# Kernel tuning notes

Measured on AMD Instinct MI355X. Metric: run time of the kernel, lower is better.

The kernel has to match this reference:

```python
import jax, jax.numpy as jnp
import numpy as np

NUM_GRAPHS = 512

def gcn_conv(x, W, b, src, dst, num_nodes):
    # PyG GCNConv: h = x @ W; add self-loops; symmetric norm D^-1/2 A D^-1/2; + bias
    h = x @ W  # [N, F]
    ones = jnp.ones(src.shape[0], dtype=x.dtype)
    deg = jax.ops.segment_sum(ones, dst, num_segments=num_nodes) + 1.0  # +1 for self-loop
    dinv = jax.lax.rsqrt(deg)  # deg >= 1 always
    coef = dinv[src] * dinv[dst]  # [E]
    msg = h[src] * coef[:, None]  # [E, F]  (dominant memory traffic)
    agg = jax.ops.segment_sum(msg, dst, num_segments=num_nodes)
    agg = agg + h * (dinv * dinv)[:, None]  # self-loop term, norm = dinv_i^2
    return agg + b

def global_mean_pool(x, batch, num_graphs):
    s = jax.ops.segment_sum(x, batch, num_segments=num_graphs)
    cnt = jax.ops.segment_sum(jnp.ones(x.shape[0], dtype=x.dtype), batch, num_segments=num_graphs)
    return s / jnp.maximum(cnt, 1.0)[:, None]

def setup_inputs() -> dict:
    key = jax.random.key(0)
    ks = jax.random.split(key, 8)
    N, E, D, H, C = 100000, 3200000, 128, 64, 2
    x = jax.random.normal(ks[0], (N, D), dtype=jnp.float32)
    edge_index = jax.random.randint(ks[1], (2, E), 0, N, dtype=jnp.int32)
    batch = jnp.sort(jax.random.randint(ks[2], (N,), 0, NUM_GRAPHS, dtype=jnp.int32))
    W1 = jax.random.normal(ks[3], (D, H), dtype=jnp.float32) / np.sqrt(D)
    b1 = jnp.zeros((H,), dtype=jnp.float32)
    W2 = jax.random.normal(ks[4], (H, H), dtype=jnp.float32) / np.sqrt(H)
    b2 = jnp.zeros((H,), dtype=jnp.float32)
    Wlin = jax.random.normal(ks[5], (H, C), dtype=jnp.float32) / np.sqrt(H)
    blin = jnp.zeros((C,), dtype=jnp.float32)
    return {"x": x, "edge_index": edge_index, "batch": batch,
            "W1": W1, "b1": b1, "W2": W2, "b2": b2, "Wlin": Wlin, "blin": blin}

def reference(x, edge_index, batch, W1, b1, W2, b2, Wlin, blin):
    # Dropout is identity at inference; omitted for a deterministic reference.
    num_nodes = x.shape[0]
    src, dst = edge_index[0], edge_index[1]
    h = jax.nn.relu(gcn_conv(x, W1, b1, src, dst, num_nodes))
    h = jax.nn.relu(gcn_conv(h, W2, b2, src, dst, num_nodes))
    g = global_mean_pool(h, batch, NUM_GRAPHS)  # [G, H]
    return g @ Wlin + blin  # [G, 2]
```

## Files before the change

kernel.cpp:

```cpp
#include <hip/hip_runtime.h>

#define HF 64
typedef unsigned short bfraw;

__device__ __forceinline__ float bf2f(bfraw u) {
    return __uint_as_float((unsigned)u << 16);
}
__device__ __forceinline__ bfraw f2bf(float f) {
    unsigned u = __float_as_uint(f);
    unsigned r = (u + 0x7FFFu + ((u >> 16) & 1u)) >> 16;
    return (bfraw)r;
}

__global__ void hist_kernel(const int* __restrict__ dst, int* __restrict__ deg, int E) {
    int e = blockIdx.x * blockDim.x + threadIdx.x;
    if (e < E) atomicAdd(&deg[dst[e]], 1);
}

__global__ __launch_bounds__(256) void scan_partial(const int* __restrict__ deg,
                                                    int* __restrict__ blocksum, int N) {
    __shared__ int red[256];
    int base = blockIdx.x * 1024 + threadIdx.x * 4;
    int s = 0;
#pragma unroll
    for (int j = 0; j < 4; ++j) {
        int i = base + j;
        if (i < N) s += deg[i];
    }
    red[threadIdx.x] = s;
    __syncthreads();
    for (int o = 128; o > 0; o >>= 1) {
        if (threadIdx.x < o) red[threadIdx.x] += red[threadIdx.x + o];
        __syncthreads();
    }
    if (threadIdx.x == 0) blocksum[blockIdx.x] = red[0];
}

__global__ __launch_bounds__(256) void scan_blocksums(int* __restrict__ blocksum, int nb) {
    __shared__ int lds[256];
    int t = threadIdx.x;
    int v = (t < nb) ? blocksum[t] : 0;
    lds[t] = v;
    __syncthreads();
    for (int o = 1; o < 256; o <<= 1) {
        int add = (t >= o) ? lds[t - o] : 0;
        __syncthreads();
        lds[t] += add;
        __syncthreads();
    }
    if (t < nb) blocksum[t] = lds[t] - v;
}

__global__ __launch_bounds__(256) void scan_apply(const int* __restrict__ deg,
                                                  const int* __restrict__ blocksum,
                                                  int* __restrict__ cursor,
                                                  float* __restrict__ dinv, int N) {
    __shared__ int lds[256];
    int base = blockIdx.x * 1024 + threadIdx.x * 4;
    int v[4];
    int s = 0;
#pragma unroll
    for (int j = 0; j < 4; ++j) {
        int i = base + j;
        v[j] = (i < N) ? deg[i] : 0;
        s += v[j];
    }
    lds[threadIdx.x] = s;
    __syncthreads();
    for (int o = 1; o < 256; o <<= 1) {
        int add = (threadIdx.x >= o) ? lds[threadIdx.x - o] : 0;
        __syncthreads();
        lds[threadIdx.x] += add;
        __syncthreads();
    }
    int run = blocksum[blockIdx.x] + lds[threadIdx.x] - s;
#pragma unroll
    for (int j = 0; j < 4; ++j) {
        int i = base + j;
        if (i < N) {
            cursor[i] = run;
            dinv[i] = rsqrtf((float)v[j] + 1.0f);
            run += v[j];
        }
    }
}

__global__ void fill_kernel(const int* __restrict__ src, const int* __restrict__ dst,
                            int* __restrict__ cursor, int* __restrict__ csr_src, int E) {
    int e = blockIdx.x * blockDim.x + threadIdx.x;
    if (e < E) {
        int d = dst[e];
        int pos = atomicAdd(&cursor[d], 1);
        csr_src[pos] = src[e];
    }
}

template <int K>
__global__ __launch_bounds__(256) void gemm_scale_f32_kernel(const float* __restrict__ X,
                                                             const float* __restrict__ W,
                                                             const float* __restrict__ scale,
                                                             bfraw* __restrict__ Y, int N) {
    __shared__ float Wl[K * HF];
    __shared__ float xs[32 * K];
    for (int i = threadIdx.x; i < K * HF; i += 256) Wl[i] = W[i];

    int node0 = blockIdx.x * 32;
    const float4* X4 = (const float4*)(X + (size_t)node0 * K);
    float4* xs4 = (float4*)xs;
    int totalf4 = 32 * K / 4;
    for (int i = threadIdx.x; i < totalf4; i += 256) {
        int n = i / (K / 4);
        if (node0 + n < N) xs4[i] = X4[i];
    }
    __syncthreads();

    int wave = threadIdx.x >> 6, f = threadIdx.x & 63;
    for (int n = wave; n < 32; n += 4) {
        int node = node0 + n;
        if (node >= N) break;
        const float4* xr = (const float4*)&xs[n * K];
        float acc = 0.0f;
#pragma unroll
        for (int k4 = 0; k4 < K / 4; ++k4) {
            float4 xv = xr[k4];
            acc += xv.x * Wl[(k4 * 4 + 0) * HF + f];
            acc += xv.y * Wl[(k4 * 4 + 1) * HF + f];
            acc += xv.z * Wl[(k4 * 4 + 2) * HF + f];
            acc += xv.w * Wl[(k4 * 4 + 3) * HF + f];
        }
        Y[(size_t)node * HF + f] = f2bf(acc * scale[node]);
    }
}

__global__ __launch_bounds__(256) void gemm_scale_bf16_kernel(const bfraw* __restrict__ X,
                                                              const float* __restrict__ W,
                                                              const float* __restrict__ scale,
                                                              bfraw* __restrict__ Y, int N) {
    __shared__ float Wl[HF * HF];
    __shared__ float xs[32 * HF];
    for (int i = threadIdx.x; i < HF * HF; i += 256) Wl[i] = W[i];

    int node0 = blockIdx.x * 32;
    const ushort4* X4 = (const ushort4*)(X + (size_t)node0 * HF);
    for (int i = threadIdx.x; i < 32 * HF / 4; i += 256) {
        int n = i >> 4;
        if (node0 + n < N) {
            ushort4 u = X4[i];
            float4 fv = make_float4(bf2f(u.x), bf2f(u.y), bf2f(u.z), bf2f(u.w));
            ((float4*)xs)[i] = fv;
        }
    }
    __syncthreads();

    int wave = threadIdx.x >> 6, f = threadIdx.x & 63;
    for (int n = wave; n < 32; n += 4) {
        int node = node0 + n;
        if (node >= N) break;
        const float4* xr = (const float4*)&xs[n * HF];
        float acc = 0.0f;
#pragma unroll
        for (int k4 = 0; k4 < HF / 4; ++k4) {
            float4 xv = xr[k4];
            acc += xv.x * Wl[(k4 * 4 + 0) * HF + f];
            acc += xv.y * Wl[(k4 * 4 + 1) * HF + f];
            acc += xv.z * Wl[(k4 * 4 + 2) * HF + f];
            acc += xv.w * Wl[(k4 * 4 + 3) * HF + f];
        }
        Y[(size_t)node * HF + f] = f2bf(acc * scale[node]);
    }
}

__device__ __forceinline__ float edge_gather_sum(const bfraw* __restrict__ hs,
                                                 const int* __restrict__ csr_src,
                                                 int beg, int end, int f) {
    float acc = 0.0f;
    for (int base = beg; base < end; base += 32) {
        int li = base + (f & 31);
        int myidx = csr_src[li < end ? li : beg];
        int rem = end - base;
#pragma unroll
        for (int j = 0; j < 32; ++j) {
            int s = __builtin_amdgcn_readlane(myidx, j);
            float v = bf2f(hs[(size_t)s * HF + f]);
            acc += (j < rem) ? v : 0.0f;
        }
    }
    return acc;
}

__global__ __launch_bounds__(256) void agg_relu_kernel(const bfraw* __restrict__ hs,
                                                       const int* __restrict__ cursor,
                                                       const int* __restrict__ deg,
                                                       const int* __restrict__ csr_src,
                                                       const float* __restrict__ dinv,
                                                       const float* __restrict__ b,
                                                       bfraw* __restrict__ out, int N) {
    int d = blockIdx.x * 4 + (threadIdx.x >> 6);
    if (d >= N) return;
    int f = threadIdx.x & 63;
    int end = cursor[d];
    int beg = end - deg[d];
    float acc = edge_gather_sum(hs, csr_src, beg, end, f);
    float self = bf2f(hs[(size_t)d * HF + f]);
    float v = dinv[d] * (acc + self) + b[f];
    out[(size_t)d * HF + f] = f2bf(fmaxf(v, 0.0f));
}

__global__ __launch_bounds__(256) void agg_pool_kernel(const bfraw* __restrict__ hs,
                                                       const int* __restrict__ cursor,
                                                       const int* __restrict__ deg,
                                                       const int* __restrict__ csr_src,
                                                       const float* __restrict__ dinv,
                                                       const float* __restrict__ b,
                                                       const int* __restrict__ batch,
                                                       float* __restrict__ pool,
                                                       float* __restrict__ cnt, int N) {
    int d = blockIdx.x * 4 + (threadIdx.x >> 6);
    if (d >= N) return;
    int f = threadIdx.x & 63;
    int end = cursor[d];
    int beg = end - deg[d];
    float acc = edge_gather_sum(hs, csr_src, beg, end, f);
    float self = bf2f(hs[(size_t)d * HF + f]);
    float v = fmaxf(dinv[d] * (acc + self) + b[f], 0.0f);
    int g = batch[d];
    atomicAdd(&pool[g * HF + f], v);
    if (f == 0) atomicAdd(&cnt[g], 1.0f);
}

__global__ void final_kernel(const float* __restrict__ pool, const float* __restrict__ cnt,
                             const float* __restrict__ Wlin, const float* __restrict__ blin,
                             float* __restrict__ out) {
    int g = blockIdx.x;
    int f = threadIdx.x;
    float v = pool[g * HF + f] / fmaxf(cnt[g], 1.0f);
    float s0 = v * Wlin[f * 2 + 0];
    float s1 = v * Wlin[f * 2 + 1];
#pragma unroll
    for (int off = 32; off > 0; off >>= 1) {
        s0 += __shfl_down(s0, off);
        s1 += __shfl_down(s1, off);
    }
    if (f == 0) {
        out[g * 2 + 0] = s0 + blin[0];
        out[g * 2 + 1] = s1 + blin[1];
    }
}

extern "C" void kernel_launch(void* const* d_in, const int* in_sizes, int n_in,
                              void* d_out, int out_size, void* d_ws, size_t ws_size,
                              hipStream_t stream) {
    const float* x    = (const float*)d_in[0];
    const int*   ei   = (const int*)d_in[1];
    const int*   bat  = (const int*)d_in[2];
    const float* W1   = (const float*)d_in[3];
    const float* b1   = (const float*)d_in[4];
    const float* W2   = (const float*)d_in[5];
    const float* b2   = (const float*)d_in[6];
    const float* Wlin = (const float*)d_in[7];
    const float* blin = (const float*)d_in[8];

    const int N = in_sizes[2];
    const int E = in_sizes[1] / 2;
    const int G = out_size / 2;
    const int* src  = ei;
    const int* dstv = ei + E;

    int*   deg      = (int*)d_ws;
    int*   cursor   = deg + N;
    int*   blocksum = cursor + N;
    int*   csr_src  = blocksum + 256;
    float* dinv     = (float*)(csr_src + E);
    float* pool     = dinv + N;
    float* cnt      = pool + (size_t)G * HF;
    uintptr_t p = (uintptr_t)(cnt + G);
    p = (p + 15) & ~(uintptr_t)15;
    bfraw* bufT = (bfraw*)p;
    bfraw* bufH = bufT + (size_t)N * HF;

    int nb = (N + 1023) / 1024;

    hipMemsetAsync(deg, 0, (size_t)N * sizeof(int), stream);
    hist_kernel<<<(E + 255) / 256, 256, 0, stream>>>(dstv, deg, E);
    scan_partial<<<nb, 256, 0, stream>>>(deg, blocksum, N);
    scan_blocksums<<<1, 256, 0, stream>>>(blocksum, nb);
    scan_apply<<<nb, 256, 0, stream>>>(deg, blocksum, cursor, dinv, N);
    fill_kernel<<<(E + 255) / 256, 256, 0, stream>>>(src, dstv, cursor, csr_src, E);

    gemm_scale_f32_kernel<128><<<(N + 31) / 32, 256, 0, stream>>>(x, W1, dinv, bufT, N);
    agg_relu_kernel<<<(N + 3) / 4, 256, 0, stream>>>(bufT, cursor, deg, csr_src, dinv, b1,
                                                     bufH, N);

    gemm_scale_bf16_kernel<<<(N + 31) / 32, 256, 0, stream>>>(bufH, W2, dinv, bufT, N);
    hipMemsetAsync(pool, 0, ((size_t)G * HF + G) * sizeof(float), stream);
    agg_pool_kernel<<<(N + 3) / 4, 256, 0, stream>>>(bufT, cursor, deg, csr_src, dinv, b2,
                                                     bat, pool, cnt, N);

    final_kernel<<<G, HF, 0, stream>>>(pool, cnt, Wlin, blin, (float*)d_out);
}
```

Before: 976.5 us.

## Partition CSR fill by destination range and batch gather loads before summing

The CSR fill kernel now launches 8 groups of blocks. Each group reads every edge but only handles edges whose destination falls in its eighth of the node range. This keeps the atomics and scattered writes confined to a smaller address window, which should improve locality, probably in the XCD-local caches. In the aggregation gather, full 32-edge chunks now issue all 32 loads into a register array before accumulating, and the masked tail is split into its own path so more loads can be in flight. The cost is that dst is read 8 times in the fill, plus extra register pressure in the gather.

```diff
diff --git a/kernel.cpp b/kernel.cpp
--- a/kernel.cpp
+++ b/kernel.cpp
@@ -85,13 +85,21 @@
     }
 }
 
-__global__ void fill_kernel(const int* __restrict__ src, const int* __restrict__ dst,
-                            int* __restrict__ cursor, int* __restrict__ csr_src, int E) {
-    int e = blockIdx.x * blockDim.x + threadIdx.x;
-    if (e < E) {
+__global__ __launch_bounds__(256) void fill_kernel(const int* __restrict__ src,
+                                                   const int* __restrict__ dst,
+                                                   int* __restrict__ cursor,
+                                                   int* __restrict__ csr_src,
+                                                   int E, int part, int nblk) {
+    int p = blockIdx.x & 7;
+    int blk = blockIdx.x >> 3;
+    int plo = p * part;
+    int phi = plo + part;
+    for (int e = blk * 256 + threadIdx.x; e < E; e += nblk * 256) {
         int d = dst[e];
-        int pos = atomicAdd(&cursor[d], 1);
-        csr_src[pos] = src[e];
+        if (d >= plo && d < phi) {
+            int pos = atomicAdd(&cursor[d], 1);
+            csr_src[pos] = src[e];
+        }
     }
 }
 
@@ -174,16 +182,30 @@
                                                  const int* __restrict__ csr_src,
                                                  int beg, int end, int f) {
     float acc = 0.0f;
-    for (int base = beg; base < end; base += 32) {
-        int li = base + (f & 31);
-        int myidx = csr_src[li < end ? li : beg];
-        int rem = end - base;
+    int base = beg;
+    for (; base + 32 <= end; base += 32) {
+        int myidx = csr_src[base + (f & 31)];
+        float v[32];
 #pragma unroll
         for (int j = 0; j < 32; ++j) {
             int s = __builtin_amdgcn_readlane(myidx, j);
-            float v = bf2f(hs[(size_t)s * HF + f]);
-            acc += (j < rem) ? v : 0.0f;
-        }
+            v[j] = bf2f(hs[(size_t)s * HF + f]);
+        }
+#pragma unroll
+        for (int j = 0; j < 32; ++j) acc += v[j];
+    }
+    if (base < end) {
+        int li = base + (f & 31);
+        int myidx = csr_src[li < end ? li : base];
+        int rem = end - base;
+        float v[32];
+#pragma unroll
+        for (int j = 0; j < 32; ++j) {
+            int s = __builtin_amdgcn_readlane(myidx, j);
+            v[j] = bf2f(hs[(size_t)s * HF + f]);
+        }
+#pragma unroll
+        for (int j = 0; j < 32; ++j) acc += (j < rem) ? v[j] : 0.0f;
     }
     return acc;
 }
@@ -285,7 +307,9 @@
     scan_partial<<<nb, 256, 0, stream>>>(deg, blocksum, N);
     scan_blocksums<<<1, 256, 0, stream>>>(blocksum, nb);
     scan_apply<<<nb, 256, 0, stream>>>(deg, blocksum, cursor, dinv, N);
-    fill_kernel<<<(E + 255) / 256, 256, 0, stream>>>(src, dstv, cursor, csr_src, E);
+    const int part = (N + 7) / 8;
+    const int nblk = 512;
+    fill_kernel<<<8 * nblk, 256, 0, stream>>>(src, dstv, cursor, csr_src, E, part, nblk);
 
     gemm_scale_f32_kernel<128><<<(N + 31) / 32, 256, 0, stream>>>(x, W1, dinv, bufT, N);
     agg_relu_kernel<<<(N + 3) / 4, 256, 0, stream>>>(bufT, cursor, deg, csr_src, dinv, b1,
```

Measured after the change: 809.4 us. 1.21x faster.
